# Optimization experiments

Hardware: AMD Instinct MI355X
Metric: run time of the kernel (lower is better)

## Reference

```python
import jax, jax.numpy as jnp
import numpy as np

HIDDEN = 512
N_CLASSES = 10

def setup_inputs() -> dict:
    key = jax.random.key(0)
    ks = jax.random.split(key, 7)
    B, T, H = 256, 784, HIDDEN
    s_ih = 1.0 / np.sqrt(H)
    inputs = jax.random.normal(ks[0], (B, T), dtype=jnp.float32)
    # nn.LSTMCell(1, H) parameters, gate order i, f, g, o
    W_ih = jax.random.uniform(ks[1], (4 * H, 1), jnp.float32, -s_ih, s_ih)
    W_hh = jax.random.uniform(ks[2], (4 * H, H), jnp.float32, -s_ih, s_ih)
    b_ih = jax.random.uniform(ks[3], (4 * H,), jnp.float32, -s_ih, s_ih)
    b_hh = jax.random.uniform(ks[4], (4 * H,), jnp.float32, -s_ih, s_ih)
    # nn.Linear(H, 10)
    W_lin = jax.random.uniform(ks[5], (N_CLASSES, H), jnp.float32, -s_ih, s_ih)
    b_lin = jax.random.uniform(ks[6], (N_CLASSES,), jnp.float32, -s_ih, s_ih)
    return {"inputs": inputs, "W_ih": W_ih, "W_hh": W_hh, "b_ih": b_ih,
            "b_hh": b_hh, "W_lin": W_lin, "b_lin": b_lin}

def reference(inputs, W_ih, W_hh, b_ih, b_hh, W_lin, b_lin):
    B = inputs.shape[0]
    H = W_hh.shape[1]
    w_in = W_ih[:, 0]          # [4H], input feature dim is 1
    bias = b_ih + b_hh         # [4H]

    def step(carry, x_t):
        h, c = carry
        # gates: [B, 4H] = x contribution + recurrent matmul + bias
        gates = x_t[:, None] * w_in[None, :] + h @ W_hh.T + bias
        i, f, g, o = jnp.split(gates, 4, axis=1)
        c_new = jax.nn.sigmoid(f) * c + jax.nn.sigmoid(i) * jnp.tanh(g)
        h_new = jax.nn.sigmoid(o) * jnp.tanh(c_new)
        return (h_new, c_new), None

    h0 = jnp.zeros((B, H), dtype=inputs.dtype)
    c0 = jnp.zeros((B, H), dtype=inputs.dtype)
    (h_T, _), _ = jax.lax.scan(step, (h0, c0), inputs.T)  # scan over T
    return h_T @ W_lin.T + b_lin  # [B, n_classes]
```

## Files before the change

### kernel.cpp

```cpp
#include <hip/hip_runtime.h>
#include <hip/hip_bf16.h>
#include <cmath>

#define HID 512
#define TSTEPS 784
#define BATCH 256
#define NCLS 10
#define NBLK 256
#define GRP 16
#define NGRP 16

typedef __bf16 bf16x8 __attribute__((ext_vector_type(8)));
typedef float f32x4 __attribute__((ext_vector_type(4)));
typedef float f32x2 __attribute__((ext_vector_type(2)));
typedef int   i32x4 __attribute__((ext_vector_type(4)));

#define SWS(r) (((unsigned)(r) & 7u) << 4)

#define LDX4_CC(dst, addr) \
    asm volatile("global_load_dwordx4 %0, %1, off sc0 sc1" : "=v"(dst) : "v"(addr) : "memory")
#define STOREDW_CC(addr, val) \
    asm volatile("global_store_dword %0, %1, off sc0 sc1" :: "v"(addr), "v"(val) : "memory")

__device__ __forceinline__ i32x4 ldflags_cc(const unsigned* a) {
    i32x4 d;
    asm volatile("global_load_dwordx4 %0, %1, off sc0 sc1\n\ts_waitcnt vmcnt(0)"
                 : "=v"(d) : "v"(a) : "memory");
    return d;
}

__global__ void init_all(const float* __restrict__ x, float* __restrict__ xT,
                         uint4* __restrict__ hz, unsigned* __restrict__ flg) {
    int t = blockIdx.x, tid = threadIdx.x;
    xT[t * BATCH + tid] = x[tid * TSTEPS + t];
    int i = t * 256 + tid;
    if (i < (512 << 10) / 16) hz[i] = make_uint4(0u, 0u, 0u, 0u);
    if (i < NGRP * 64) flg[i] = 0u;
}

__device__ __forceinline__ float sigmoid_f(float v) {
    return __fdividef(1.f, 1.f + __expf(-v));
}
__device__ __forceinline__ float tanh_f(float v) {
    float e = __expf(fminf(fmaxf(2.f * v, -30.f), 30.f));
    return __fdividef(e - 1.f, e + 1.f);
}

__global__ __launch_bounds__(512)
void lstm_persist(const float* __restrict__ xT,
                  const float* __restrict__ W_hh,
                  const float* __restrict__ w_in,
                  const float* __restrict__ b_ih,
                  const float* __restrict__ b_hh,
                  __bf16* __restrict__ h0,
                  __bf16* __restrict__ h1,
                  float* __restrict__ hf,
                  unsigned* __restrict__ flg)
{
    __shared__ __align__(16) __bf16 wlds[128 * HID];
    __shared__ __align__(16) __bf16 hlds[16 * HID];
    __shared__ float gl[4][16][33];
    __shared__ float xl[16];

    const int tid  = threadIdx.x;
    const int lane = tid & 63;
    const int w    = tid >> 6;
    const int s    = w & 3;
    const int ch   = w >> 2;
    const int bg   = blockIdx.x >> 4;
    const int cs   = blockIdx.x & 15;
    const int b0   = bg * 16;
    const int j0   = cs * 32;
    const int rlo  = lane & 15;
    const int khi  = (lane >> 4) * 8;

    unsigned* flags = flg + bg * 64;

    {
        int r = tid >> 2;
        int q = tid & 3;
        int gs = r >> 5, jj = r & 31;
        const float* src = W_hh + (size_t)(gs * HID + j0 + jj) * HID + q * 128;
        char* wp = (char*)wlds;
        unsigned rowb = (unsigned)r * (HID * 2);
        unsigned sw   = SWS(r);
        #pragma unroll
        for (int cc = 0; cc < 128; cc += 8) {
            float4 va = *(const float4*)(src + cc);
            float4 vb = *(const float4*)(src + cc + 4);
            bf16x8 pk;
            pk[0]=(__bf16)va.x; pk[1]=(__bf16)va.y; pk[2]=(__bf16)va.z; pk[3]=(__bf16)va.w;
            pk[4]=(__bf16)vb.x; pk[5]=(__bf16)vb.y; pk[6]=(__bf16)vb.z; pk[7]=(__bf16)vb.w;
            *(bf16x8*)(wp + ((rowb + (unsigned)(q * 128 + cc) * 2) ^ sw)) = pk;
        }
    }

    const int Rc = tid >> 4;
    const int c2 = (tid & 15) * 2;
    float win_r[4][2], bias_r[4][2];
    #pragma unroll
    for (int g = 0; g < 4; ++g)
        #pragma unroll
        for (int ii = 0; ii < 2; ++ii) {
            int idx = g * HID + j0 + c2 + ii;
            win_r[g][ii]  = w_in[idx];
            bias_r[g][ii] = b_ih[idx] + b_hh[idx];
        }
    float creg[2] = {0.f, 0.f};

    const int rS  = tid & 15;
    const int seg = tid >> 4;
    const unsigned rowbS = (unsigned)rS * (HID * 2);
    const unsigned swS   = SWS(rS);

    const unsigned rBb = (unsigned)(s * 32 + ch * 16 + rlo) * (HID * 2);
    const unsigned swB = SWS(rlo);
    const char* wbp = (const char*)wlds;
    const char* hbp = (const char*)hlds;
    char* hwp = (char*)hlds;

    __syncthreads();

    for (int t = 0; t < TSTEPS; ++t) {
        const __bf16* hprev = (t & 1) ? h1 : h0;
        __bf16* hnext       = (t & 1) ? h0 : h1;

        {
            const __bf16* gsrc = hprev + (size_t)(b0 + rS) * HID + seg * 16;
            i32x4 t0, t1;
            LDX4_CC(t0, gsrc);
            LDX4_CC(t1, gsrc + 8);
            asm volatile("s_waitcnt vmcnt(0)" ::: "memory");
            __builtin_amdgcn_sched_barrier(0);
            unsigned base = rowbS + (unsigned)seg * 32u;
            *(i32x4*)(hwp + ((base +  0u) ^ swS)) = t0;
            *(i32x4*)(hwp + ((base + 16u) ^ swS)) = t1;
        }
        if (tid < 16) xl[tid] = xT[t * BATCH + b0 + tid];
        __syncthreads();

        f32x4 acc0 = {0.f,0.f,0.f,0.f};
        #pragma unroll
        for (int ks = 0; ks < 16; ++ks) {
            unsigned colb = (unsigned)(khi * 2 + ks * 64);
            bf16x8 a0 = *(const bf16x8*)(hbp + (((unsigned)rlo * 1024u + colb) ^ SWS(rlo)));
            bf16x8 b  = *(const bf16x8*)(wbp + ((rBb + colb) ^ swB));
            acc0 = __builtin_amdgcn_mfma_f32_16x16x32_bf16(a0, b, acc0, 0, 0, 0);
        }
        #pragma unroll
        for (int rr = 0; rr < 4; ++rr) {
            int rowl = (lane >> 4) * 4 + rr;
            gl[s][rowl][ch * 16 + rlo] = acc0[rr];
        }
        __syncthreads();

        if (tid < 256) {
            float xv = xl[Rc];
            float hn2[2];
            #pragma unroll
            for (int ii = 0; ii < 2; ++ii) {
                int ccx = c2 + ii;
                float gi = gl[0][Rc][ccx] + xv * win_r[0][ii] + bias_r[0][ii];
                float gf = gl[1][Rc][ccx] + xv * win_r[1][ii] + bias_r[1][ii];
                float gg = gl[2][Rc][ccx] + xv * win_r[2][ii] + bias_r[2][ii];
                float go = gl[3][Rc][ccx] + xv * win_r[3][ii] + bias_r[3][ii];
                float cn = sigmoid_f(gf) * creg[ii] + sigmoid_f(gi) * tanh_f(gg);
                creg[ii] = cn;
                hn2[ii]  = sigmoid_f(go) * tanh_f(cn);
            }
            union { __bf16 b[2]; int i; } u;
            u.b[0] = (__bf16)hn2[0]; u.b[1] = (__bf16)hn2[1];
            __bf16* dst = hnext + (size_t)(b0 + Rc) * HID + j0 + c2;
            STOREDW_CC(dst, u.i);
            if (t == TSTEPS - 1)
                *(f32x2*)(hf + (size_t)(b0 + Rc) * HID + j0 + c2) = (f32x2){hn2[0], hn2[1]};
        }

        if (t == TSTEPS - 1) break;

        asm volatile("s_waitcnt vmcnt(0)" ::: "memory");
        __syncthreads();
        unsigned tgt = (unsigned)(t + 1);
        if (tid == 0) STOREDW_CC(flags + cs, (int)tgt);
        if (tid < 4) {
            const unsigned* fp = flags + tid * 4;
            int bad;
            do {
                __builtin_amdgcn_s_sleep(1);
                i32x4 f = ldflags_cc(fp);
                bad = ((unsigned)f[0] < tgt) | ((unsigned)f[1] < tgt) |
                      ((unsigned)f[2] < tgt) | ((unsigned)f[3] < tgt);
            } while (__any(bad));
        }
        __syncthreads();
    }
}

__global__ void head(const float* __restrict__ hfp, const float* __restrict__ Wl,
                     const float* __restrict__ bl_, float* __restrict__ out)
{
    __shared__ float hr[HID];
    int b = blockIdx.x;
    for (int k = threadIdx.x; k < HID; k += blockDim.x) hr[k] = hfp[b * HID + k];
    __syncthreads();
    int j = threadIdx.x;
    if (j < NCLS) {
        float acc = bl_[j];
        for (int k = 0; k < HID; ++k) acc += hr[k] * Wl[j * HID + k];
        out[b * NCLS + j] = acc;
    }
}

extern "C" void kernel_launch(void* const* d_in, const int* in_sizes, int n_in,
                              void* d_out, int out_size, void* d_ws, size_t ws_size,
                              hipStream_t stream) {
    const float* inputs = (const float*)d_in[0];
    const float* W_ih   = (const float*)d_in[1];
    const float* W_hh   = (const float*)d_in[2];
    const float* b_ih   = (const float*)d_in[3];
    const float* b_hh   = (const float*)d_in[4];
    const float* W_lin  = (const float*)d_in[5];
    const float* b_lin  = (const float*)d_in[6];

    const size_t OFS_H1  = 256u << 10;
    const size_t OFS_HF  = 512u << 10;
    const size_t OFS_XT  = 1024u << 10;
    const size_t OFS_FLG = OFS_XT + (size_t)TSTEPS * BATCH * 4;
    const size_t NEEDED  = OFS_FLG + NGRP * 64 * 4;
    if (ws_size < NEEDED) return;

    char* ws = (char*)d_ws;
    __bf16* h0 = (__bf16*)ws;
    __bf16* h1 = (__bf16*)(ws + OFS_H1);
    float*  hf = (float*)(ws + OFS_HF);
    float*  xT = (float*)(ws + OFS_XT);
    unsigned* flg = (unsigned*)(ws + OFS_FLG);

    init_all<<<TSTEPS, BATCH, 0, stream>>>(inputs, xT, (uint4*)h0, flg);

    lstm_persist<<<NBLK, 512, 0, stream>>>(xT, W_hh, W_ih, b_ih, b_hh,
                                           h0, h1, hf, flg);

    head<<<BATCH, 64, 0, stream>>>(hf, W_lin, b_lin, (float*)d_out);
}
```

Measured before the change: 2.884 ms.

## Replace flag barrier with tag-embedded hidden state polling between blocks

Drops the per-step flag array and inter-block barrier. Each hidden value is now stored as an fp32 word whose top 16 bits carry the bf16 value and whose low 8 bits carry a step tag. Consumers spin on the hidden-state loads until every tag matches the current step, then pack the bf16 halves into LDS. This removes a separate flag store, flag poll and extra __syncthreads round trip on each recurrent step. In exchange it doubles the bytes of h moved per step and relies on the tag low bits never colliding across the two alternating buffers.

```diff
diff --git a/kernel.cpp b/kernel.cpp
--- a/kernel.cpp
+++ b/kernel.cpp
@@ -7,35 +7,27 @@
 #define BATCH 256
 #define NCLS 10
 #define NBLK 256
-#define GRP 16
 #define NGRP 16
 
 typedef __bf16 bf16x8 __attribute__((ext_vector_type(8)));
 typedef float f32x4 __attribute__((ext_vector_type(4)));
 typedef float f32x2 __attribute__((ext_vector_type(2)));
 typedef int   i32x4 __attribute__((ext_vector_type(4)));
+typedef int   i32x2 __attribute__((ext_vector_type(2)));
 
 #define SWS(r) (((unsigned)(r) & 7u) << 4)
 
 #define LDX4_CC(dst, addr) \
     asm volatile("global_load_dwordx4 %0, %1, off sc0 sc1" : "=v"(dst) : "v"(addr) : "memory")
-#define STOREDW_CC(addr, val) \
-    asm volatile("global_store_dword %0, %1, off sc0 sc1" :: "v"(addr), "v"(val) : "memory")
-
-__device__ __forceinline__ i32x4 ldflags_cc(const unsigned* a) {
-    i32x4 d;
-    asm volatile("global_load_dwordx4 %0, %1, off sc0 sc1\n\ts_waitcnt vmcnt(0)"
-                 : "=v"(d) : "v"(a) : "memory");
-    return d;
-}
+#define STX2_CC(addr, val) \
+    asm volatile("global_store_dwordx2 %0, %1, off sc0 sc1" :: "v"(addr), "v"(val) : "memory")
 
 __global__ void init_all(const float* __restrict__ x, float* __restrict__ xT,
-                         uint4* __restrict__ hz, unsigned* __restrict__ flg) {
+                         uint4* __restrict__ hz) {
     int t = blockIdx.x, tid = threadIdx.x;
     xT[t * BATCH + tid] = x[tid * TSTEPS + t];
     int i = t * 256 + tid;
-    if (i < (512 << 10) / 16) hz[i] = make_uint4(0u, 0u, 0u, 0u);
-    if (i < NGRP * 64) flg[i] = 0u;
+    if (i < (1 << 20) / 16) hz[i] = make_uint4(0u, 0u, 0u, 0u);
 }
 
 __device__ __forceinline__ float sigmoid_f(float v) {
@@ -52,10 +44,9 @@
                   const float* __restrict__ w_in,
                   const float* __restrict__ b_ih,
                   const float* __restrict__ b_hh,
-                  __bf16* __restrict__ h0,
-                  __bf16* __restrict__ h1,
-                  float* __restrict__ hf,
-                  unsigned* __restrict__ flg)
+                  float* __restrict__ h0,
+                  float* __restrict__ h1,
+                  float* __restrict__ hf)
 {
     __shared__ __align__(16) __bf16 wlds[128 * HID];
     __shared__ __align__(16) __bf16 hlds[16 * HID];
@@ -74,8 +65,6 @@
     const int rlo  = lane & 15;
     const int khi  = (lane >> 4) * 8;
 
-    unsigned* flags = flg + bg * 64;
-
     {
         int r = tid >> 2;
         int q = tid & 3;
@@ -122,19 +111,41 @@
     __syncthreads();
 
     for (int t = 0; t < TSTEPS; ++t) {
-        const __bf16* hprev = (t & 1) ? h1 : h0;
-        __bf16* hnext       = (t & 1) ? h0 : h1;
+        const float* hprev = (t & 1) ? h1 : h0;
+        float* hnext       = (t & 1) ? h0 : h1;
 
         {
-            const __bf16* gsrc = hprev + (size_t)(b0 + rS) * HID + seg * 16;
-            i32x4 t0, t1;
-            LDX4_CC(t0, gsrc);
-            LDX4_CC(t1, gsrc + 8);
-            asm volatile("s_waitcnt vmcnt(0)" ::: "memory");
+            const float* gsrc = hprev + (size_t)(b0 + rS) * HID + seg * 16;
+            const unsigned tag = (unsigned)(t & 0xFF);
+            i32x4 v0, v1, v2, v3;
+            for (;;) {
+                LDX4_CC(v0, gsrc);     LDX4_CC(v1, gsrc + 4);
+                LDX4_CC(v2, gsrc + 8); LDX4_CC(v3, gsrc + 12);
+                asm volatile("s_waitcnt vmcnt(0)" ::: "memory");
+                unsigned bad = 0;
+                #pragma unroll
+                for (int k = 0; k < 4; ++k) {
+                    bad |= ((unsigned)v0[k] ^ tag) & 0xFFu;
+                    bad |= ((unsigned)v1[k] ^ tag) & 0xFFu;
+                    bad |= ((unsigned)v2[k] ^ tag) & 0xFFu;
+                    bad |= ((unsigned)v3[k] ^ tag) & 0xFFu;
+                }
+                if (!bad) break;
+                __builtin_amdgcn_s_sleep(1);
+            }
             __builtin_amdgcn_sched_barrier(0);
+            i32x4 o0, o1;
+            o0[0] = (int)(((unsigned)v0[0] >> 16) | ((unsigned)v0[1] & 0xFFFF0000u));
+            o0[1] = (int)(((unsigned)v0[2] >> 16) | ((unsigned)v0[3] & 0xFFFF0000u));
+            o0[2] = (int)(((unsigned)v1[0] >> 16) | ((unsigned)v1[1] & 0xFFFF0000u));
+            o0[3] = (int)(((unsigned)v1[2] >> 16) | ((unsigned)v1[3] & 0xFFFF0000u));
+            o1[0] = (int)(((unsigned)v2[0] >> 16) | ((unsigned)v2[1] & 0xFFFF0000u));
+            o1[1] = (int)(((unsigned)v2[2] >> 16) | ((unsigned)v2[3] & 0xFFFF0000u));
+            o1[2] = (int)(((unsigned)v3[0] >> 16) | ((unsigned)v3[1] & 0xFFFF0000u));
+            o1[3] = (int)(((unsigned)v3[2] >> 16) | ((unsigned)v3[3] & 0xFFFF0000u));
             unsigned base = rowbS + (unsigned)seg * 32u;
-            *(i32x4*)(hwp + ((base +  0u) ^ swS)) = t0;
-            *(i32x4*)(hwp + ((base + 16u) ^ swS)) = t1;
+            *(i32x4*)(hwp + ((base +  0u) ^ swS)) = o0;
+            *(i32x4*)(hwp + ((base + 16u) ^ swS)) = o1;
         }
         if (tid < 16) xl[tid] = xT[t * BATCH + b0 + tid];
         __syncthreads();
@@ -168,29 +179,19 @@
                 creg[ii] = cn;
                 hn2[ii]  = sigmoid_f(go) * tanh_f(cn);
             }
-            union { __bf16 b[2]; int i; } u;
-            u.b[0] = (__bf16)hn2[0]; u.b[1] = (__bf16)hn2[1];
-            __bf16* dst = hnext + (size_t)(b0 + Rc) * HID + j0 + c2;
-            STOREDW_CC(dst, u.i);
-            if (t == TSTEPS - 1)
+            if (t == TSTEPS - 1) {
                 *(f32x2*)(hf + (size_t)(b0 + Rc) * HID + j0 + c2) = (f32x2){hn2[0], hn2[1]};
-        }
-
-        if (t == TSTEPS - 1) break;
-
-        asm volatile("s_waitcnt vmcnt(0)" ::: "memory");
-        __syncthreads();
-        unsigned tgt = (unsigned)(t + 1);
-        if (tid == 0) STOREDW_CC(flags + cs, (int)tgt);
-        if (tid < 4) {
-            const unsigned* fp = flags + tid * 4;
-            int bad;
-            do {
-                __builtin_amdgcn_s_sleep(1);
-                i32x4 f = ldflags_cc(fp);
-                bad = ((unsigned)f[0] < tgt) | ((unsigned)f[1] < tgt) |
-                      ((unsigned)f[2] < tgt) | ((unsigned)f[3] < tgt);
-            } while (__any(bad));
+            } else {
+                const unsigned tagn = (unsigned)((t + 1) & 0xFF);
+                union { float f; unsigned u; } a0u, a1u;
+                a0u.f = (float)(__bf16)hn2[0];
+                a1u.f = (float)(__bf16)hn2[1];
+                i32x2 st;
+                st[0] = (int)(a0u.u | tagn);
+                st[1] = (int)(a1u.u | tagn);
+                float* dst = hnext + (size_t)(b0 + Rc) * HID + j0 + c2;
+                STX2_CC(dst, st);
+            }
         }
         __syncthreads();
     }
@@ -222,24 +223,22 @@
     const float* W_lin  = (const float*)d_in[5];
     const float* b_lin  = (const float*)d_in[6];
 
-    const size_t OFS_H1  = 256u << 10;
-    const size_t OFS_HF  = 512u << 10;
-    const size_t OFS_XT  = 1024u << 10;
-    const size_t OFS_FLG = OFS_XT + (size_t)TSTEPS * BATCH * 4;
-    const size_t NEEDED  = OFS_FLG + NGRP * 64 * 4;
+    const size_t OFS_H1 = 512u << 10;
+    const size_t OFS_HF = 1024u << 10;
+    const size_t OFS_XT = 1536u << 10;
+    const size_t NEEDED = OFS_XT + (size_t)TSTEPS * BATCH * 4;
     if (ws_size < NEEDED) return;
 
     char* ws = (char*)d_ws;
-    __bf16* h0 = (__bf16*)ws;
-    __bf16* h1 = (__bf16*)(ws + OFS_H1);
-    float*  hf = (float*)(ws + OFS_HF);
-    float*  xT = (float*)(ws + OFS_XT);
-    unsigned* flg = (unsigned*)(ws + OFS_FLG);
-
-    init_all<<<TSTEPS, BATCH, 0, stream>>>(inputs, xT, (uint4*)h0, flg);
+    float* h0 = (float*)ws;
+    float* h1 = (float*)(ws + OFS_H1);
+    float* hf = (float*)(ws + OFS_HF);
+    float* xT = (float*)(ws + OFS_XT);
+
+    init_all<<<TSTEPS, BATCH, 0, stream>>>(inputs, xT, (uint4*)ws);
 
     lstm_persist<<<NBLK, 512, 0, stream>>>(xT, W_hh, W_ih, b_ih, b_hh,
-                                           h0, h1, hf, flg);
+                                           h0, h1, hf);
 
     head<<<BATCH, 64, 0, stream>>>(hf, W_lin, b_lin, (float*)d_out);
 }
```

Measured after the change: 3.145 ms. 1.09x slower.

## Interleave two batch groups per block to hide inter-block sync latency

Applied to the files above, without the earlier changes.

Halves the persistent grid so each block handles two 16-row batch groups, alternating between them within each timestep. Each phase now signals the other group's flags, so one group's cross-block handshake overlaps the other group's MFMA and gate work. The full block-wide poll-and-barrier is replaced by a single-dword flag poll done by every thread just before it loads its h slice. The cost is that half as many CUs are used and each block does twice the serial work per step, and the new flag protocol relies on the vmcnt wait in the next phase to order the h stores before the flag is published.

```diff
diff --git a/kernel.cpp b/kernel.cpp
--- a/kernel.cpp
+++ b/kernel.cpp
@@ -6,8 +6,7 @@
 #define TSTEPS 784
 #define BATCH 256
 #define NCLS 10
-#define NBLK 256
-#define GRP 16
+#define NBLK 128
 #define NGRP 16
 
 typedef __bf16 bf16x8 __attribute__((ext_vector_type(8)));
@@ -22,9 +21,9 @@
 #define STOREDW_CC(addr, val) \
     asm volatile("global_store_dword %0, %1, off sc0 sc1" :: "v"(addr), "v"(val) : "memory")
 
-__device__ __forceinline__ i32x4 ldflags_cc(const unsigned* a) {
-    i32x4 d;
-    asm volatile("global_load_dwordx4 %0, %1, off sc0 sc1\n\ts_waitcnt vmcnt(0)"
+__device__ __forceinline__ unsigned lddw_cc_wait(const unsigned* a) {
+    unsigned d;
+    asm volatile("global_load_dword %0, %1, off sc0 sc1\n\ts_waitcnt vmcnt(0)"
                  : "=v"(d) : "v"(a) : "memory");
     return d;
 }
@@ -60,21 +59,23 @@
     __shared__ __align__(16) __bf16 wlds[128 * HID];
     __shared__ __align__(16) __bf16 hlds[16 * HID];
     __shared__ float gl[4][16][33];
-    __shared__ float xl[16];
+    __shared__ float xl2[2][16];
 
     const int tid  = threadIdx.x;
     const int lane = tid & 63;
     const int w    = tid >> 6;
     const int s    = w & 3;
     const int ch   = w >> 2;
-    const int bg   = blockIdx.x >> 4;
+    const int p    = blockIdx.x >> 4;
     const int cs   = blockIdx.x & 15;
-    const int b0   = bg * 16;
+    const int b0A  = (p * 2) * 16;
+    const int b0B  = (p * 2 + 1) * 16;
     const int j0   = cs * 32;
     const int rlo  = lane & 15;
     const int khi  = (lane >> 4) * 8;
 
-    unsigned* flags = flg + bg * 64;
+    unsigned* flagsA = flg + (p * 2) * 64;
+    unsigned* flagsB = flg + (p * 2 + 1) * 64;
 
     {
         int r = tid >> 2;
@@ -106,7 +107,7 @@
             win_r[g][ii]  = w_in[idx];
             bias_r[g][ii] = b_ih[idx] + b_hh[idx];
         }
-    float creg[2] = {0.f, 0.f};
+    float cregA[2] = {0.f, 0.f}, cregB[2] = {0.f, 0.f};
 
     const int rS  = tid & 15;
     const int seg = tid >> 4;
@@ -121,23 +122,25 @@
 
     __syncthreads();
 
-    for (int t = 0; t < TSTEPS; ++t) {
-        const __bf16* hprev = (t & 1) ? h1 : h0;
-        __bf16* hnext       = (t & 1) ? h0 : h1;
-
+    auto phase = [&](int t, int b0, const __bf16* hprev, __bf16* hnext,
+                     unsigned* fpoll, unsigned* fstore, unsigned sval,
+                     float (&creg)[2], float* xlp) {
         {
+            const unsigned* fp = fpoll + (seg >> 1);
+            while (lddw_cc_wait(fp) < (unsigned)t) __builtin_amdgcn_s_sleep(1);
             const __bf16* gsrc = hprev + (size_t)(b0 + rS) * HID + seg * 16;
-            i32x4 t0, t1;
-            LDX4_CC(t0, gsrc);
-            LDX4_CC(t1, gsrc + 8);
+            i32x4 v0, v1;
+            LDX4_CC(v0, gsrc);
+            LDX4_CC(v1, gsrc + 8);
             asm volatile("s_waitcnt vmcnt(0)" ::: "memory");
             __builtin_amdgcn_sched_barrier(0);
             unsigned base = rowbS + (unsigned)seg * 32u;
-            *(i32x4*)(hwp + ((base +  0u) ^ swS)) = t0;
-            *(i32x4*)(hwp + ((base + 16u) ^ swS)) = t1;
-        }
-        if (tid < 16) xl[tid] = xT[t * BATCH + b0 + tid];
+            *(i32x4*)(hwp + ((base +  0u) ^ swS)) = v0;
+            *(i32x4*)(hwp + ((base + 16u) ^ swS)) = v1;
+            if (tid < 16) xlp[tid] = xT[t * BATCH + b0 + tid];
+        }
         __syncthreads();
+        if (tid == 0) STOREDW_CC(fstore + cs, (int)sval);
 
         f32x4 acc0 = {0.f,0.f,0.f,0.f};
         #pragma unroll
@@ -155,7 +158,7 @@
         __syncthreads();
 
         if (tid < 256) {
-            float xv = xl[Rc];
+            float xv = xlp[Rc];
             float hn2[2];
             #pragma unroll
             for (int ii = 0; ii < 2; ++ii) {
@@ -168,31 +171,22 @@
                 creg[ii] = cn;
                 hn2[ii]  = sigmoid_f(go) * tanh_f(cn);
             }
-            union { __bf16 b[2]; int i; } u;
-            u.b[0] = (__bf16)hn2[0]; u.b[1] = (__bf16)hn2[1];
-            __bf16* dst = hnext + (size_t)(b0 + Rc) * HID + j0 + c2;
-            STOREDW_CC(dst, u.i);
-            if (t == TSTEPS - 1)
+            if (t == TSTEPS - 1) {
                 *(f32x2*)(hf + (size_t)(b0 + Rc) * HID + j0 + c2) = (f32x2){hn2[0], hn2[1]};
-        }
-
-        if (t == TSTEPS - 1) break;
-
-        asm volatile("s_waitcnt vmcnt(0)" ::: "memory");
-        __syncthreads();
-        unsigned tgt = (unsigned)(t + 1);
-        if (tid == 0) STOREDW_CC(flags + cs, (int)tgt);
-        if (tid < 4) {
-            const unsigned* fp = flags + tid * 4;
-            int bad;
-            do {
-                __builtin_amdgcn_s_sleep(1);
-                i32x4 f = ldflags_cc(fp);
-                bad = ((unsigned)f[0] < tgt) | ((unsigned)f[1] < tgt) |
-                      ((unsigned)f[2] < tgt) | ((unsigned)f[3] < tgt);
-            } while (__any(bad));
-        }
-        __syncthreads();
+            } else {
+                union { __bf16 b[2]; int i; } u;
+                u.b[0] = (__bf16)hn2[0]; u.b[1] = (__bf16)hn2[1];
+                __bf16* dst = hnext + (size_t)(b0 + Rc) * HID + j0 + c2;
+                STOREDW_CC(dst, u.i);
+            }
+        }
+    };
+
+    for (int t = 0; t < TSTEPS; ++t) {
+        const __bf16* hprev = (t & 1) ? h1 : h0;
+        __bf16* hnext       = (t & 1) ? h0 : h1;
+        phase(t, b0A, hprev, hnext, flagsA, flagsB, (unsigned)t, cregA, xl2[0]);
+        phase(t, b0B, hprev, hnext, flagsB, flagsA, (unsigned)(t + 1), cregB, xl2[1]);
     }
 }
 
```

Measured after the change: 4.062 ms. +40.9%, slower.
